# Kernel tuning notes

Measured on AMD Instinct MI355X. Metric: run time of the kernel, lower is better.

## Reference

```python
import jax, jax.numpy as jnp
import numpy as np

STRIDE = 1

def setup_inputs() -> dict:
    key = jax.random.key(0)
    k1, k2, k3 = jax.random.split(key, 3)
    x = jax.random.normal(k1, (32, 64, 112, 112), dtype=jnp.float32)
    weight = jax.random.normal(k2, (128, 64, 3, 3), dtype=jnp.float32)
    bias = jax.random.normal(k3, (128,), dtype=jnp.float32)
    return {"x": x, "weight": weight, "bias": bias}

def reference(x, weight, bias):
    # Naive per-patch multiply-sum conv == standard cross-correlation conv2d,
    # stride=1, no padding (VALID).  x: (N,Cin,H,W), weight: (Cout,Cin,kH,kW)
    out = jax.lax.conv_general_dilated(
        x, weight,
        window_strides=(STRIDE, STRIDE),
        padding="VALID",
        dimension_numbers=("NCHW", "OIHW", "NCHW"),
    )
    return out + bias[None, :, None, None]
```

## Files before the change

kernel.cpp:

```cpp
#include <hip/hip_runtime.h>
#include <hip/hip_bf16.h>


#define CIN   64
#define COUT  128
#define INH   112
#define INW   112
#define OUTH  110
#define OUTW  110
#define NB    32
#define KTOT  576
#define NPIX  (NB*OUTH*OUTW)

typedef __attribute__((ext_vector_type(8))) short short8;
typedef __attribute__((ext_vector_type(4))) float f32x4;
typedef __attribute__((ext_vector_type(4))) unsigned int uint4v;

static __device__ __forceinline__ unsigned short f2bf(float f) {
    union { float f; unsigned int u; } v; v.f = f;
    return (unsigned short)((v.u + 0x7FFF + ((v.u >> 16) & 1)) >> 16);
}

__global__ __launch_bounds__(256) void convert_x(const float* __restrict__ x,
                                                 unsigned short* __restrict__ xhwc) {
    __shared__ unsigned short lds[64 * 117];
    const int h = blockIdx.x;
    const int n = blockIdx.y;
    const int t = threadIdx.x;
    const float* xp = x + ((size_t)n * CIN) * (INH * INW) + (size_t)h * INW;
#pragma unroll
    for (int i = 0; i < 28; ++i) {
        int f = t + 256 * i;
        int ci = f / 112, w = f - ci * 112;
        lds[ci * 117 + w] = f2bf(xp[(size_t)ci * (INH * INW) + w]);
    }
    __syncthreads();
    unsigned int* dst = (unsigned int*)(xhwc + ((size_t)(n * INH + h) * INW) * 64);
#pragma unroll
    for (int i = 0; i < 14; ++i) {
        int g = t + 256 * i;
        int w = g >> 5, cp = g & 31;
        unsigned int lo = lds[(cp * 2) * 117 + w];
        unsigned int hi = lds[(cp * 2 + 1) * 117 + w];
        dst[g] = lo | (hi << 16);
    }
}

__global__ __launch_bounds__(256) void prepack_w(const float* __restrict__ w,
                                                 unsigned short* __restrict__ ap) {
    int flat = blockIdx.x * 256 + threadIdx.x;
    int m = flat / KTOT;
    int k = flat - m * KTOT;
    int khw = k >> 6, ci = k & 63;
    int kh = khw / 3, kw = khw - kh * 3;
    float v = w[((m * CIN + ci) * 3 + kh) * 3 + kw];
    ap[((k >> 3) * COUT + m) * 8 + (k & 7)] = f2bf(v);
}

__global__ __launch_bounds__(256) void conv_gemm(const unsigned short* __restrict__ xhwc,
                                                 const unsigned short* __restrict__ ap,
                                                 const float* __restrict__ bias,
                                                 float* __restrict__ out) {
    __shared__ unsigned short ldsB[25600];
    const int oh = blockIdx.x;
    const int n  = blockIdx.y;
    const int t  = threadIdx.x;

    {
        const uint4v* src = (const uint4v*)(xhwc + ((size_t)(n * INH + oh) * INW) * 64);
        for (int c = t; c < 2688; c += 256) {
            int kh = c / 896;
            int r  = c - kh * 896;
            int w_ = r >> 3, part = r & 7;
            *(uint4v*)&ldsB[(kh * INW + w_) * 72 + part * 8] = src[c];
        }
    }
    __syncthreads();

    const int lane = t & 63;
    const int wave = t >> 6;
    const int m_base  = (wave >> 1) * 64;
    const int px_base = (wave & 1) * 64;
    const int l16  = lane & 15;
    const int quad = lane >> 4;

    f32x4 acc[4][4] = {};
    const short8* A = (const short8*)ap;

    for (int kc = 0; kc < 18; ++kc) {
        const int khw = kc >> 1;
        const int kh = khw / 3, kw = khw - kh * 3;
        const int ci0 = (kc & 1) * 32 + quad * 8;
        short8 a[4], b[4];
#pragma unroll
        for (int i = 0; i < 4; ++i)
            a[i] = A[(kc * 4 + quad) * COUT + (m_base + i * 16 + l16)];
#pragma unroll
        for (int j = 0; j < 4; ++j) {
            int ow = px_base + j * 16 + l16;
            b[j] = *(const short8*)&ldsB[(kh * INW + ow + kw) * 72 + ci0];
        }
#pragma unroll
        for (int i = 0; i < 4; ++i)
#pragma unroll
            for (int j = 0; j < 4; ++j)
                acc[i][j] = __builtin_amdgcn_mfma_f32_16x16x32_bf16(a[i], b[j], acc[i][j], 0, 0, 0);
    }

#pragma unroll
    for (int i = 0; i < 4; ++i) {
        const int co = m_base + i * 16 + quad * 4;
#pragma unroll
        for (int j = 0; j < 4; ++j) {
            const int ow = px_base + j * 16 + l16;
            if (ow < OUTW) {
                const size_t ob = (((size_t)n * COUT + co) * OUTH + oh) * OUTW + ow;
#pragma unroll
                for (int r = 0; r < 4; ++r)
                    out[ob + (size_t)r * (OUTH * OUTW)] = acc[i][j][r] + bias[co + r];
            }
        }
    }
}

#define TCO 16
__global__ __launch_bounds__(256) void conv_direct(const float* __restrict__ x,
                                                   const float* __restrict__ w,
                                                   const float* __restrict__ bias,
                                                   float* __restrict__ out) {
    int p = blockIdx.x * 256 + threadIdx.x;
    const int co0 = blockIdx.y * TCO;
    const bool valid = p < NPIX;
    if (!valid) p = 0;
    const int n = p / (OUTH * OUTW);
    const int rem = p - n * (OUTH * OUTW);
    const int oh = rem / OUTW;
    const int ow = rem - oh * OUTW;
    float acc[TCO];
#pragma unroll
    for (int t = 0; t < TCO; ++t) acc[t] = bias[co0 + t];
    const float* xb = x + ((size_t)n * CIN) * (INH * INW) + (size_t)oh * INW + ow;
    const float* wb = w + (size_t)co0 * CIN * 9;
    for (int ci = 0; ci < CIN; ++ci) {
        const float* xp = xb + (size_t)ci * (INH * INW);
        const float* wp = wb + ci * 9;
#pragma unroll
        for (int kh = 0; kh < 3; ++kh) {
            const float x0 = xp[kh * INW + 0];
            const float x1 = xp[kh * INW + 1];
            const float x2 = xp[kh * INW + 2];
#pragma unroll
            for (int t = 0; t < TCO; ++t) {
                const float* wt = wp + t * (CIN * 9) + kh * 3;
                acc[t] = fmaf(x0, wt[0], acc[t]);
                acc[t] = fmaf(x1, wt[1], acc[t]);
                acc[t] = fmaf(x2, wt[2], acc[t]);
            }
        }
    }
    if (valid) {
        const size_t ob = ((size_t)n * COUT + co0) * (OUTH * OUTW) + (size_t)oh * OUTW + ow;
#pragma unroll
        for (int t = 0; t < TCO; ++t)
            out[ob + (size_t)t * (OUTH * OUTW)] = acc[t];
    }
}

extern "C" void kernel_launch(void* const* d_in, const int* in_sizes, int n_in,
                              void* d_out, int out_size, void* d_ws, size_t ws_size,
                              hipStream_t stream) {
    const float* x    = (const float*)d_in[0];
    const float* w    = (const float*)d_in[1];
    const float* bias = (const float*)d_in[2];
    float* out        = (float*)d_out;

    const size_t xhwc_bytes = (size_t)NB * INH * INW * 64 * 2;
    const size_t ap_bytes   = (size_t)COUT * KTOT * 2;

    if (ws_size >= xhwc_bytes + ap_bytes) {
        unsigned short* xhwc = (unsigned short*)d_ws;
        unsigned short* apck = (unsigned short*)((char*)d_ws + xhwc_bytes);
        convert_x<<<dim3(INH, NB), 256, 0, stream>>>(x, xhwc);
        prepack_w<<<288, 256, 0, stream>>>(w, apck);
        conv_gemm<<<dim3(OUTH, NB), 256, 0, stream>>>(xhwc, apck, bias, out);
    } else {
        dim3 grid((NPIX + 255) / 256, COUT / TCO);
        conv_direct<<<grid, dim3(256), 0, stream>>>(x, w, bias, out);
    }
}
```

Measured before the change: 367.7 us.

## Double-buffer A/B fragments in conv GEMM and vectorize input conversion loads

```diff
diff --git a/kernel.cpp b/kernel.cpp
--- a/kernel.cpp
+++ b/kernel.cpp
@@ -15,6 +15,7 @@
 typedef __attribute__((ext_vector_type(8))) short short8;
 typedef __attribute__((ext_vector_type(4))) float f32x4;
 typedef __attribute__((ext_vector_type(4))) unsigned int uint4v;
+typedef __attribute__((ext_vector_type(2))) unsigned int uint2v;
 
 static __device__ __forceinline__ unsigned short f2bf(float f) {
     union { float f; unsigned int u; } v; v.f = f;
@@ -23,16 +24,20 @@
 
 __global__ __launch_bounds__(256) void convert_x(const float* __restrict__ x,
                                                  unsigned short* __restrict__ xhwc) {
-    __shared__ unsigned short lds[64 * 117];
+    __shared__ unsigned short lds[64 * 116];
     const int h = blockIdx.x;
     const int n = blockIdx.y;
     const int t = threadIdx.x;
     const float* xp = x + ((size_t)n * CIN) * (INH * INW) + (size_t)h * INW;
 #pragma unroll
-    for (int i = 0; i < 28; ++i) {
+    for (int i = 0; i < 7; ++i) {
         int f = t + 256 * i;
-        int ci = f / 112, w = f - ci * 112;
-        lds[ci * 117 + w] = f2bf(xp[(size_t)ci * (INH * INW) + w]);
+        int ci = f / 28, w4 = f - ci * 28;
+        f32x4 v = *(const f32x4*)(xp + (size_t)ci * (INH * INW) + 4 * w4);
+        uint2v d;
+        d[0] = (unsigned int)f2bf(v[0]) | ((unsigned int)f2bf(v[1]) << 16);
+        d[1] = (unsigned int)f2bf(v[2]) | ((unsigned int)f2bf(v[3]) << 16);
+        *(uint2v*)&lds[ci * 116 + 4 * w4] = d;
     }
     __syncthreads();
     unsigned int* dst = (unsigned int*)(xhwc + ((size_t)(n * INH + h) * INW) * 64);
@@ -40,8 +45,8 @@
     for (int i = 0; i < 14; ++i) {
         int g = t + 256 * i;
         int w = g >> 5, cp = g & 31;
-        unsigned int lo = lds[(cp * 2) * 117 + w];
-        unsigned int hi = lds[(cp * 2 + 1) * 117 + w];
+        unsigned int lo = lds[(cp * 2) * 116 + w];
+        unsigned int hi = lds[(cp * 2 + 1) * 116 + w];
         dst[g] = lo | (hi << 16);
     }
 }
@@ -57,14 +62,42 @@
     ap[((k >> 3) * COUT + m) * 8 + (k & 7)] = f2bf(v);
 }
 
-__global__ __launch_bounds__(256) void conv_gemm(const unsigned short* __restrict__ xhwc,
-                                                 const unsigned short* __restrict__ ap,
-                                                 const float* __restrict__ bias,
-                                                 float* __restrict__ out) {
+__global__ __launch_bounds__(256, 3) void conv_gemm(const unsigned short* __restrict__ xhwc,
+                                                    const unsigned short* __restrict__ ap,
+                                                    const float* __restrict__ bias,
+                                                    float* __restrict__ out) {
     __shared__ unsigned short ldsB[25600];
     const int oh = blockIdx.x;
     const int n  = blockIdx.y;
     const int t  = threadIdx.x;
+
+    const int lane = t & 63;
+    const int wave = t >> 6;
+    const int m_base  = (wave >> 1) * 64;
+    const int px_base = (wave & 1) * 64;
+    const int l16  = lane & 15;
+    const int quad = lane >> 4;
+
+    const short8* A = (const short8*)ap;
+
+    auto loadA = [&](short8* a, int kc) {
+#pragma unroll
+        for (int i = 0; i < 4; ++i)
+            a[i] = A[(kc * 4 + quad) * COUT + (m_base + i * 16 + l16)];
+    };
+    auto loadB = [&](short8* b, int kc) {
+        const int khw = kc >> 1;
+        const int kh = khw / 3, kw = khw - kh * 3;
+        const int ci0 = (kc & 1) * 32 + quad * 8;
+#pragma unroll
+        for (int j = 0; j < 4; ++j) {
+            int ow = px_base + j * 16 + l16;
+            b[j] = *(const short8*)&ldsB[(kh * INW + ow + kw) * 72 + ci0];
+        }
+    };
+
+    short8 a0[4], a1[4], b0[4], b1[4];
+    loadA(a0, 0);
 
     {
         const uint4v* src = (const uint4v*)(xhwc + ((size_t)(n * INH + oh) * INW) * 64);
@@ -75,36 +108,27 @@
             *(uint4v*)&ldsB[(kh * INW + w_) * 72 + part * 8] = src[c];
         }
     }
+    loadA(a1, 1);
     __syncthreads();
 
-    const int lane = t & 63;
-    const int wave = t >> 6;
-    const int m_base  = (wave >> 1) * 64;
-    const int px_base = (wave & 1) * 64;
-    const int l16  = lane & 15;
-    const int quad = lane >> 4;
-
     f32x4 acc[4][4] = {};
-    const short8* A = (const short8*)ap;
-
-    for (int kc = 0; kc < 18; ++kc) {
-        const int khw = kc >> 1;
-        const int kh = khw / 3, kw = khw - kh * 3;
-        const int ci0 = (kc & 1) * 32 + quad * 8;
-        short8 a[4], b[4];
+    loadB(b0, 0);
+    loadB(b1, 1);
+
+#pragma unroll
+    for (int kc = 0; kc < 18; kc += 2) {
 #pragma unroll
         for (int i = 0; i < 4; ++i)
-            a[i] = A[(kc * 4 + quad) * COUT + (m_base + i * 16 + l16)];
-#pragma unroll
-        for (int j = 0; j < 4; ++j) {
-            int ow = px_base + j * 16 + l16;
-            b[j] = *(const short8*)&ldsB[(kh * INW + ow + kw) * 72 + ci0];
-        }
+#pragma unroll
+            for (int j = 0; j < 4; ++j)
+                acc[i][j] = __builtin_amdgcn_mfma_f32_16x16x32_bf16(a0[i], b0[j], acc[i][j], 0, 0, 0);
+        if (kc + 2 < 18) { loadA(a0, kc + 2); loadB(b0, kc + 2); }
 #pragma unroll
         for (int i = 0; i < 4; ++i)
 #pragma unroll
             for (int j = 0; j < 4; ++j)
-                acc[i][j] = __builtin_amdgcn_mfma_f32_16x16x32_bf16(a[i], b[j], acc[i][j], 0, 0, 0);
+                acc[i][j] = __builtin_amdgcn_mfma_f32_16x16x32_bf16(a1[i], b1[j], acc[i][j], 0, 0, 0);
+        if (kc + 3 < 18) { loadA(a1, kc + 3); loadB(b1, kc + 3); }
     }
 
 #pragma unroll
```

After: 364.4 us. No clear change (-0.9%).
